# Kernel optimization log

Measured on AMD Instinct MI355X. Metric: run time of the kernel, lower is better.

## Reference

```python
import jax, jax.numpy as jnp
import numpy as np

D_IN = 2048; D_OUT = 2048; DL = 512; NUM_HEAD = 16; CTX = 2048
HEAD_DIM = D_OUT // NUM_HEAD  # 128


def setup_inputs() -> dict:
    key = jax.random.key(0)
    ks = jax.random.split(key, 20)
    s = 0.02
    def lin(k, din, dout):
        k1, k2 = jax.random.split(k)
        return (jax.random.normal(k1, (din, dout), jnp.float32) * s,
                jax.random.normal(k2, (dout,), jnp.float32) * s)
    w_kv, b_kv = lin(ks[0], D_IN, DL)
    w_ku, b_ku = lin(ks[1], DL, D_OUT // 2)
    w_kr, b_kr = lin(ks[2], D_IN, D_OUT // 2)
    w_vu, b_vu = lin(ks[3], DL, D_OUT)
    w_q,  b_q  = lin(ks[4], D_IN, DL)
    w_qu, b_qu = lin(ks[5], DL, D_OUT // 2)
    w_qr, b_qr = lin(ks[6], DL, D_OUT // 2)
    w_o,  b_o  = lin(ks[7], D_OUT, D_OUT)
    x = jax.random.normal(ks[8], (2, 2048, D_IN), jnp.float32)
    return dict(x=x, w_kv=w_kv, b_kv=b_kv, w_ku=w_ku, b_ku=b_ku, w_kr=w_kr, b_kr=b_kr,
                w_vu=w_vu, b_vu=b_vu, w_q=w_q, b_q=b_q, w_qu=w_qu, b_qu=b_qu,
                w_qr=w_qr, b_qr=b_qr, w_o=w_o, b_o=b_o)


def reference(x, w_kv, b_kv, w_ku, b_ku, w_kr, b_kr, w_vu, b_vu,
              w_q, b_q, w_qu, b_qu, w_qr, b_qr, w_o, b_o):
    b, s, _ = x.shape
    # latent KV compression
    ckv = x @ w_kv + b_kv                                   # (b, s, dl)
    # NOTE: source Rope.forward is a no-op (returns input), replicated faithfully.
    key = jnp.concatenate([ckv @ w_ku + b_ku, x @ w_kr + b_kr], axis=-1)   # (b, s, d_out)
    q_lat = x @ w_q + b_q                                   # (b, s, dl)
    query = jnp.concatenate([q_lat @ w_qu + b_qu, q_lat @ w_qr + b_qr], axis=-1)
    value = ckv @ w_vu + b_vu                               # (b, s, d_out)
    # split heads -> (b, h, s, hd)
    def heads(t):
        return t.reshape(b, s, NUM_HEAD, HEAD_DIM).transpose(0, 2, 1, 3)
    q, k, v = heads(query), heads(key), heads(value)
    scores = jnp.einsum('bhqd,bhkd->bhqk', q, k)
    causal = jnp.tril(jnp.ones((s, s), dtype=bool))
    scores = jnp.where(causal, scores, -jnp.inf)
    at = jax.nn.softmax(scores / jnp.sqrt(jnp.float32(HEAD_DIM)), axis=-1)
    # dropout rate 0 -> identity
    out = jnp.einsum('bhqk,bhkd->bhqd', at, v).transpose(0, 2, 1, 3).reshape(b, s, D_OUT)
    return out @ w_o + b_o
```

## Files before the change

### kernel.cpp

```cpp
#include <hip/hip_runtime.h>
#include <hip/hip_bf16.h>

typedef __hip_bfloat16 bf16;
typedef __bf16 bf16_t;
typedef __bf16 bf16x8 __attribute__((ext_vector_type(8)));
typedef __bf16 bf16x4v __attribute__((ext_vector_type(4)));
typedef float f32x4 __attribute__((ext_vector_type(4)));

#define D_IN 2048
#define D_OUT 2048
#define DL 512
#define NUM_HEAD 16
#define SEQ 2048
#define HEAD_DIM 128
#define BATCH 2
#define NTOK (BATCH * SEQ)

__device__ __forceinline__ void stf(float* p, float v) { *p = v; }
__device__ __forceinline__ void stf(bf16_t* p, float v) { *p = (bf16_t)v; }

__device__ __forceinline__ void async_cp16(const bf16_t* g, bf16_t* l) {
    __builtin_amdgcn_global_load_lds(
        (const __attribute__((address_space(1))) void*)g,
        (__attribute__((address_space(3))) void*)l, 16, 0, 0);
}

#define CVTB 8192
#define NTOPS 8

struct TOp { const float* W; bf16_t* Wt; int K, N, nx, nblk; };
struct TOps { TOp op[NTOPS]; };

__global__ __launch_bounds__(256) void prep_kernel(
    const float* __restrict__ x, bf16_t* __restrict__ xb,
    TOps ops,
    const float* __restrict__ b_kv, const float* __restrict__ b_q,
    float* __restrict__ bkvq,
    const float* __restrict__ b_qu, const float* __restrict__ b_qr,
    float* __restrict__ bquqr, int trb)
{
    const int tid = threadIdx.x;
    int blk = blockIdx.x;

    if (blk < CVTB) {
        int i = (blk * 256 + tid) * 4;
        float4 v = *(const float4*)&x[i];
        bf16_t o[4] = {(bf16_t)v.x, (bf16_t)v.y, (bf16_t)v.z, (bf16_t)v.w};
        *(ulong1*)&xb[i] = *(ulong1*)o;
        return;
    }
    blk -= CVTB;
    if (blk < trb) {
        int op = 0;
        while (blk >= ops.op[op].nblk) { blk -= ops.op[op].nblk; ++op; }
        const TOp& t = ops.op[op];
        const int n0 = (blk % t.nx) * 32, k0 = (blk / t.nx) * 32;
        __shared__ float tl[32][33];
        const int c = tid & 31, r0 = tid >> 5;
#pragma unroll
        for (int rr = 0; rr < 32; rr += 8)
            tl[r0 + rr][c] = t.W[(size_t)(k0 + r0 + rr) * t.N + n0 + c];
        __syncthreads();
#pragma unroll
        for (int rr = 0; rr < 32; rr += 8)
            t.Wt[(size_t)(n0 + r0 + rr) * t.K + k0 + c] = (bf16_t)tl[c][r0 + rr];
        return;
    }
    blk -= trb;
    if (blk == 0) {
#pragma unroll
        for (int j = 0; j < 4; ++j) {
            int i = tid + j * 256;
            bkvq[i] = (i < DL) ? b_kv[i] : b_q[i - DL];
        }
    } else {
#pragma unroll
        for (int j = 0; j < 8; ++j) {
            int i = tid + j * 256;
            bquqr[i] = (i < 1024) ? b_qu[i] : b_qr[i - 1024];
        }
    }
}

struct GOp { const bf16_t* A; const bf16_t* Wt; const float* bias;
             void* C; int lda, K, col0, ldc, nx, nblk; };
template <int N> struct GOps { GOp op[N]; };

template <typename TC, int NOPS>
__global__ __launch_bounds__(256) void gemm_multi_kernel(GOps<NOPS> ops)
{
    __shared__ __align__(16) bf16_t As[2 * 128 * 32];
    __shared__ __align__(16) bf16_t Bs[2 * 128 * 32];

    int blk = blockIdx.x;
    int opi = 0;
    while (blk >= ops.op[opi].nblk) { blk -= ops.op[opi].nblk; ++opi; }
    const GOp& g = ops.op[opi];

    const int tid  = threadIdx.x;
    const int wave = tid >> 6, lane = tid & 63;
    const int quad = lane >> 4, l16 = lane & 15;
    const int wm = wave & 1, wn = wave >> 1;
    const int m0 = (blk / g.nx) * 128;
    const int n0 = (blk % g.nx) * 128;

    const int r0 = tid >> 2, c0 = (tid & 3) * 8;
    const bf16_t* Ap0 = g.A  + (size_t)(m0 + r0)      * g.lda + c0;
    const bf16_t* Ap1 = g.A  + (size_t)(m0 + r0 + 64) * g.lda + c0;
    const bf16_t* Bp0 = g.Wt + (size_t)(n0 + r0)      * g.K   + c0;
    const bf16_t* Bp1 = g.Wt + (size_t)(n0 + r0 + 64) * g.K   + c0;

    f32x4 acc[4][4];
#pragma unroll
    for (int i = 0; i < 4; ++i)
#pragma unroll
        for (int j = 0; j < 4; ++j) acc[i][j] = (f32x4){0.f, 0.f, 0.f, 0.f};

    for (int k0 = 0; k0 < g.K; k0 += 64) {
        __syncthreads();
#pragma unroll
        for (int p = 0; p < 2; ++p) {
            async_cp16(Ap0 + k0 + p * 32, As + p * 4096 + tid * 8);
            async_cp16(Ap1 + k0 + p * 32, As + p * 4096 + 2048 + tid * 8);
            async_cp16(Bp0 + k0 + p * 32, Bs + p * 4096 + tid * 8);
            async_cp16(Bp1 + k0 + p * 32, Bs + p * 4096 + 2048 + tid * 8);
        }
        __syncthreads();

#pragma unroll
        for (int p = 0; p < 2; ++p) {
            bf16x8 af[4], bfr[4];
#pragma unroll
            for (int t = 0; t < 4; ++t) {
                af[t]  = *(const bf16x8*)&As[p * 4096 + (wm * 64 + t * 16 + l16) * 32 + quad * 8];
                bfr[t] = *(const bf16x8*)&Bs[p * 4096 + (wn * 64 + t * 16 + l16) * 32 + quad * 8];
            }
#pragma unroll
            for (int mt = 0; mt < 4; ++mt)
#pragma unroll
                for (int nt = 0; nt < 4; ++nt)
                    acc[mt][nt] = __builtin_amdgcn_mfma_f32_16x16x32_bf16(
                        af[mt], bfr[nt], acc[mt][nt], 0, 0, 0);
        }
    }

    TC* C = (TC*)g.C;
    const int mrow = m0 + wm * 64 + quad * 4;
#pragma unroll
    for (int mt = 0; mt < 4; ++mt)
#pragma unroll
        for (int nt = 0; nt < 4; ++nt) {
            int col = n0 + wn * 64 + nt * 16 + l16;
            float bv = g.bias[col];
#pragma unroll
            for (int r = 0; r < 4; ++r)
                stf(&C[(size_t)(mrow + mt * 16 + r) * g.ldc + g.col0 + col],
                    acc[mt][nt][r] + bv);
        }
}

#define KS_LD 136
#define VT_LD 72

__global__ __launch_bounds__(256, 4) void attn_mfma_kernel(
    bf16_t* __restrict__ Qg, const bf16_t* __restrict__ Kg,
    const bf16_t* __restrict__ Vg)
{
    __shared__ __align__(16) bf16_t Ks[64 * KS_LD];
    __shared__ __align__(16) bf16_t Vt[128 * VT_LD];

    const int tid  = threadIdx.x;
    const int wave = tid >> 6;
    const int lane = tid & 63;
    const int quad = lane >> 4;
    const int l16  = lane & 15;

    const int grp = blockIdx.x & 31;
    const int h   = grp & 15;
    const int b   = grp >> 4;
    const int u   = blockIdx.x >> 5;
    const int ua  = u >> 3, uc = u & 7;
    const int qt  = 8 * ua + ((ua & 1) ? (7 - uc) : uc);
    const int ntiles = qt + 1;

    const int base = b * SEQ;
    const int hd0  = h * HEAD_DIM;
    const float scale = 0.08838834764831845f;

    bf16x8 qf[4];
    {
        const bf16_t* qp = Qg + (size_t)(base + qt * 64 + wave * 16 + l16) * D_OUT + hd0;
#pragma unroll
        for (int kb = 0; kb < 4; ++kb)
            qf[kb] = *(const bf16x8*)(qp + kb * 32 + quad * 8);
    }

    f32x4 o[8];
#pragma unroll
    for (int ob = 0; ob < 8; ++ob) o[ob] = (f32x4){0.f, 0.f, 0.f, 0.f};
    float m_i = -INFINITY, l_i = 0.f;

    const int rk = tid >> 4, ck = (tid & 15) * 8;
    const int kg = (tid & 15) * 4, dg = tid >> 4;
    const int rbase = (rk >> 2) * 8 + (rk & 3);

    bf16x8 kpre[4], vpre[4];
    auto issue = [&](int k0) {
        const bf16_t* kp = Kg + (size_t)(base + k0 + rbase) * D_OUT + hd0 + ck;
        kpre[0] = *(const bf16x8*)(kp);
        kpre[1] = *(const bf16x8*)(kp + (size_t)4  * D_OUT);
        kpre[2] = *(const bf16x8*)(kp + (size_t)32 * D_OUT);
        kpre[3] = *(const bf16x8*)(kp + (size_t)36 * D_OUT);
#pragma unroll
        for (int kk = 0; kk < 4; ++kk)
            vpre[kk] = *(const bf16x8*)&Vg[(size_t)(base + k0 + kg + kk) * D_OUT + hd0 + dg * 8];
    };
    issue(0);

    const int qabs = qt * 64 + wave * 16 + l16;
    const int qwav = qt * 64 + wave * 16;

    for (int t = 0; t < ntiles; ++t) {
        const int k0 = t * 64;
        __syncthreads();
#pragma unroll
        for (int jj = 0; jj < 4; ++jj)
            *(bf16x8*)&Ks[(rk + 16 * jj) * KS_LD + ck] = kpre[jj];
#pragma unroll
        for (int j = 0; j < 8; ++j) {
            bf16x4v pk = {vpre[0][j], vpre[1][j], vpre[2][j], vpre[3][j]};
            *(bf16x4v*)&Vt[(dg * 8 + j) * VT_LD + kg] = pk;
        }
        __syncthreads();
        if (t + 1 < ntiles) issue(k0 + 64);

        f32x4 s[4];
#pragma unroll
        for (int nb = 0; nb < 4; ++nb) s[nb] = (f32x4){0.f, 0.f, 0.f, 0.f};
#pragma unroll
        for (int kb = 0; kb < 4; ++kb)
#pragma unroll
            for (int nb = 0; nb < 4; ++nb) {
                bf16x8 kfrag = *(const bf16x8*)&Ks[(nb * 16 + l16) * KS_LD + kb * 32 + quad * 8];
                s[nb] = __builtin_amdgcn_mfma_f32_16x16x32_bf16(kfrag, qf[kb], s[nb], 0, 0, 0);
            }

        if (k0 + 63 <= qwav) {
#pragma unroll
            for (int nb = 0; nb < 4; ++nb)
#pragma unroll
                for (int r = 0; r < 4; ++r) s[nb][r] *= scale;
        } else {
#pragma unroll
            for (int nb = 0; nb < 4; ++nb) {
                int key = k0 + (nb >> 1) * 32 + quad * 8 + (nb & 1) * 4;
#pragma unroll
                for (int r = 0; r < 4; ++r)
                    s[nb][r] = (key + r <= qabs) ? s[nb][r] * scale : -INFINITY;
            }
        }

        float rmax = -INFINITY;
#pragma unroll
        for (int nb = 0; nb < 4; ++nb)
#pragma unroll
            for (int r = 0; r < 4; ++r) rmax = fmaxf(rmax, s[nb][r]);
        rmax = fmaxf(rmax, __shfl_xor(rmax, 16, 64));
        rmax = fmaxf(rmax, __shfl_xor(rmax, 32, 64));

        const bool defer = (bool)__all(rmax - m_i <= 8.f);
        const float mnew = defer ? m_i : fmaxf(m_i, rmax);

        float rs = 0.f;
#pragma unroll
        for (int nb = 0; nb < 4; ++nb)
#pragma unroll
            for (int r = 0; r < 4; ++r) {
                float pv = __expf(s[nb][r] - mnew);
                s[nb][r] = pv;
                rs += pv;
            }
        rs += __shfl_xor(rs, 16, 64);
        rs += __shfl_xor(rs, 32, 64);

        if (!defer) {
            const float alpha = __expf(m_i - mnew);
            l_i = l_i * alpha + rs;
            m_i = mnew;
#pragma unroll
            for (int ob = 0; ob < 8; ++ob)
#pragma unroll
                for (int r = 0; r < 4; ++r) o[ob][r] *= alpha;
        } else {
            l_i += rs;
        }

        bf16x8 pb0, pb1;
#pragma unroll
        for (int r = 0; r < 4; ++r) {
            pb0[r]     = (bf16_t)s[0][r];
            pb0[4 + r] = (bf16_t)s[1][r];
            pb1[r]     = (bf16_t)s[2][r];
            pb1[4 + r] = (bf16_t)s[3][r];
        }

#pragma unroll
        for (int ob = 0; ob < 8; ++ob) {
            bf16x8 v0 = *(const bf16x8*)&Vt[(ob * 16 + l16) * VT_LD + 0 + quad * 8];
            o[ob] = __builtin_amdgcn_mfma_f32_16x16x32_bf16(v0, pb0, o[ob], 0, 0, 0);
            bf16x8 v1 = *(const bf16x8*)&Vt[(ob * 16 + l16) * VT_LD + 32 + quad * 8];
            o[ob] = __builtin_amdgcn_mfma_f32_16x16x32_bf16(v1, pb1, o[ob], 0, 0, 0);
        }
    }

    {
        const int q = qt * 64 + wave * 16 + l16;
        const float inv = 1.f / l_i;
        bf16_t* orow = Qg + (size_t)(base + q) * D_OUT + hd0;
#pragma unroll
        for (int ob = 0; ob < 8; ++ob) {
            bf16x4v pk = {(bf16_t)(o[ob][0] * inv), (bf16_t)(o[ob][1] * inv),
                          (bf16_t)(o[ob][2] * inv), (bf16_t)(o[ob][3] * inv)};
            *(bf16x4v*)&orow[ob * 16 + quad * 4] = pk;
        }
    }
}

extern "C" void kernel_launch(void* const* d_in, const int* in_sizes, int n_in,
                              void* d_out, int out_size, void* d_ws, size_t ws_size,
                              hipStream_t stream)
{
    const float* x    = (const float*)d_in[0];
    const float* w_kv = (const float*)d_in[1];
    const float* b_kv = (const float*)d_in[2];
    const float* w_ku = (const float*)d_in[3];
    const float* b_ku = (const float*)d_in[4];
    const float* w_kr = (const float*)d_in[5];
    const float* b_kr = (const float*)d_in[6];
    const float* w_vu = (const float*)d_in[7];
    const float* b_vu = (const float*)d_in[8];
    const float* w_q  = (const float*)d_in[9];
    const float* b_q  = (const float*)d_in[10];
    const float* w_qu = (const float*)d_in[11];
    const float* b_qu = (const float*)d_in[12];
    const float* w_qr = (const float*)d_in[13];
    const float* b_qr = (const float*)d_in[14];
    const float* w_o  = (const float*)d_in[15];
    const float* b_o  = (const float*)d_in[16];
    float* out = (float*)d_out;

    bf16_t* ws    = (bf16_t*)d_ws;
    bf16_t* ckvq  = ws;
    bf16_t* query = ckvq  + NTOK * 1024;
    bf16_t* value = query + NTOK * D_OUT;
    bf16_t* wt_kv = value + NTOK * D_OUT;
    bf16_t* wt_q  = wt_kv + 512 * 2048;
    bf16_t* wt_ku = wt_q  + 512 * 2048;
    bf16_t* wt_kr = wt_ku + 1024 * 512;
    bf16_t* wt_vu = wt_kr + 1024 * 2048;
    bf16_t* wt_qu = wt_vu + 2048 * 512;
    bf16_t* wt_qr = wt_qu + 1024 * 512;
    bf16_t* wt_o  = wt_qr + 1024 * 512;
    float*  bkvq  = (float*)(wt_o + 2048 * 2048);
    float*  bquqr = bkvq + 1024;
    bf16_t* key   = (bf16_t*)d_out;
    bf16_t* xb    = key + NTOK * D_OUT;

    TOps tops = {{
        { w_kv, wt_kv, 2048,  512, 16,  16 * 64 },
        { w_q,  wt_q,  2048,  512, 16,  16 * 64 },
        { w_ku, wt_ku,  512, 1024, 32,  32 * 16 },
        { w_kr, wt_kr, 2048, 1024, 32,  32 * 64 },
        { w_vu, wt_vu,  512, 2048, 64,  64 * 16 },
        { w_qu, wt_qu,  512, 1024, 32,  32 * 16 },
        { w_qr, wt_qr,  512, 1024, 32,  32 * 16 },
        { w_o,  wt_o,  2048, 2048, 64,  64 * 64 },
    }};
    int trb = 0;
    for (int i = 0; i < NTOPS; ++i) trb += tops.op[i].nblk;
    prep_kernel<<<CVTB + trb + 2, 256, 0, stream>>>(
        x, xb, tops, b_kv, b_q, bkvq, b_qu, b_qr, bquqr, trb);

    GOps<1> s1 = {{
        { xb, wt_kv, bkvq, ckvq, D_IN, D_IN, 0, 1024, 8, 8 * 32 },
    }};
    gemm_multi_kernel<bf16_t, 1><<<8 * 32, 256, 0, stream>>>(s1);

    GOps<4> s2 = {{
        { xb,         wt_kr, b_kr,  key,   D_IN, 2048, 1024, D_OUT,  8, 256 },
        { ckvq + 512, wt_qu, bquqr, query, 1024,  512,    0, D_OUT, 16, 512 },
        { ckvq,       wt_vu, b_vu,  value, 1024,  512,    0, D_OUT, 16, 512 },
        { ckvq,       wt_ku, b_ku,  key,   1024,  512,    0, D_OUT,  8, 256 },
    }};
    gemm_multi_kernel<bf16_t, 4><<<1536, 256, 0, stream>>>(s2);

    attn_mfma_kernel<<<1024, 256, 0, stream>>>(query, key, value);

    GOps<1> s3 = {{
        { query, wt_o, b_o, out, D_OUT, 2048, 0, D_OUT, 16, 512 },
    }};
    gemm_multi_kernel<float, 1><<<512, 256, 0, stream>>>(s3);
}
```

Before: 399.2 us.

## Pair complementary query tiles per attention block, double-buffer K/V, fold scale into Q

Each attention block now processes two query tiles (p and 31-p) that share the same K/V tiles, so causal work is balanced across blocks and each loaded K/V tile feeds twice the MFMAs. K/V shared memory is double-buffered, which removes one barrier per tile, and the MFMA sections are wrapped in s_setprio. The softmax scale is folded into the query GEMM epilogue through a new per-op cscale field, removing the per-score multiply. In exchange, register pressure roughly doubles (launch bounds drop from 4 to 2 blocks per SIMD), only 512 blocks are launched, and LDS use per block doubles.

```diff
diff --git a/kernel.cpp b/kernel.cpp
--- a/kernel.cpp
+++ b/kernel.cpp
@@ -15,6 +15,10 @@
 #define HEAD_DIM 128
 #define BATCH 2
 #define NTOK (BATCH * SEQ)
+#define SCALE 0.08838834764831845f
+
+struct CTrue  { static constexpr bool value = true;  };
+struct CFalse { static constexpr bool value = false; };
 
 __device__ __forceinline__ void stf(float* p, float v) { *p = v; }
 __device__ __forceinline__ void stf(bf16_t* p, float v) { *p = (bf16_t)v; }
@@ -83,7 +87,7 @@
 }
 
 struct GOp { const bf16_t* A; const bf16_t* Wt; const float* bias;
-             void* C; int lda, K, col0, ldc, nx, nblk; };
+             void* C; int lda, K, col0, ldc, nx, nblk; float cscale; };
 template <int N> struct GOps { GOp op[N]; };
 
 template <typename TC, int NOPS>
@@ -155,19 +159,21 @@
 #pragma unroll
             for (int r = 0; r < 4; ++r)
                 stf(&C[(size_t)(mrow + mt * 16 + r) * g.ldc + g.col0 + col],
-                    acc[mt][nt][r] + bv);
+                    (acc[mt][nt][r] + bv) * g.cscale);
         }
 }
 
 #define KS_LD 136
 #define VT_LD 72
-
-__global__ __launch_bounds__(256, 4) void attn_mfma_kernel(
+#define KS_SZ (64 * KS_LD)
+#define VT_SZ (128 * VT_LD)
+
+__global__ __launch_bounds__(256, 2) void attn_mfma_kernel(
     bf16_t* __restrict__ Qg, const bf16_t* __restrict__ Kg,
     const bf16_t* __restrict__ Vg)
 {
-    __shared__ __align__(16) bf16_t Ks[64 * KS_LD];
-    __shared__ __align__(16) bf16_t Vt[128 * VT_LD];
+    __shared__ __align__(16) bf16_t Ks[2][KS_SZ];
+    __shared__ __align__(16) bf16_t Vt[2][VT_SZ];
 
     const int tid  = threadIdx.x;
     const int wave = tid >> 6;
@@ -178,27 +184,31 @@
     const int grp = blockIdx.x & 31;
     const int h   = grp & 15;
     const int b   = grp >> 4;
-    const int u   = blockIdx.x >> 5;
-    const int ua  = u >> 3, uc = u & 7;
-    const int qt  = 8 * ua + ((ua & 1) ? (7 - uc) : uc);
-    const int ntiles = qt + 1;
+    const int p   = blockIdx.x >> 5;
+    const int qtA = p, qtB = 31 - p;
+    const int ntiles = qtB + 1;
 
     const int base = b * SEQ;
     const int hd0  = h * HEAD_DIM;
-    const float scale = 0.08838834764831845f;
-
-    bf16x8 qf[4];
+
+    bf16x8 qfA[4], qfB[4];
     {
-        const bf16_t* qp = Qg + (size_t)(base + qt * 64 + wave * 16 + l16) * D_OUT + hd0;
-#pragma unroll
-        for (int kb = 0; kb < 4; ++kb)
-            qf[kb] = *(const bf16x8*)(qp + kb * 32 + quad * 8);
-    }
-
-    f32x4 o[8];
-#pragma unroll
-    for (int ob = 0; ob < 8; ++ob) o[ob] = (f32x4){0.f, 0.f, 0.f, 0.f};
-    float m_i = -INFINITY, l_i = 0.f;
+        const bf16_t* qa = Qg + (size_t)(base + qtA * 64 + wave * 16 + l16) * D_OUT + hd0;
+        const bf16_t* qb = Qg + (size_t)(base + qtB * 64 + wave * 16 + l16) * D_OUT + hd0;
+#pragma unroll
+        for (int kb = 0; kb < 4; ++kb) {
+            qfA[kb] = *(const bf16x8*)(qa + kb * 32 + quad * 8);
+            qfB[kb] = *(const bf16x8*)(qb + kb * 32 + quad * 8);
+        }
+    }
+
+    f32x4 oA[8], oB[8];
+#pragma unroll
+    for (int ob = 0; ob < 8; ++ob) {
+        oA[ob] = (f32x4){0.f, 0.f, 0.f, 0.f};
+        oB[ob] = (f32x4){0.f, 0.f, 0.f, 0.f};
+    }
+    float mA = -INFINITY, mB = -INFINITY, lA = 0.f, lB = 0.f;
 
     const int rk = tid >> 4, ck = (tid & 15) * 8;
     const int kg = (tid & 15) * 4, dg = tid >> 4;
@@ -215,51 +225,26 @@
         for (int kk = 0; kk < 4; ++kk)
             vpre[kk] = *(const bf16x8*)&Vg[(size_t)(base + k0 + kg + kk) * D_OUT + hd0 + dg * 8];
     };
-    issue(0);
-
-    const int qabs = qt * 64 + wave * 16 + l16;
-    const int qwav = qt * 64 + wave * 16;
-
-    for (int t = 0; t < ntiles; ++t) {
-        const int k0 = t * 64;
-        __syncthreads();
+
+    auto stage = [&](int buf) {
+        bf16_t* ks = Ks[buf]; bf16_t* vt = Vt[buf];
 #pragma unroll
         for (int jj = 0; jj < 4; ++jj)
-            *(bf16x8*)&Ks[(rk + 16 * jj) * KS_LD + ck] = kpre[jj];
+            *(bf16x8*)&ks[(rk + 16 * jj) * KS_LD + ck] = kpre[jj];
 #pragma unroll
         for (int j = 0; j < 8; ++j) {
             bf16x4v pk = {vpre[0][j], vpre[1][j], vpre[2][j], vpre[3][j]};
-            *(bf16x4v*)&Vt[(dg * 8 + j) * VT_LD + kg] = pk;
-        }
-        __syncthreads();
-        if (t + 1 < ntiles) issue(k0 + 64);
-
-        f32x4 s[4];
-#pragma unroll
-        for (int nb = 0; nb < 4; ++nb) s[nb] = (f32x4){0.f, 0.f, 0.f, 0.f};
-#pragma unroll
-        for (int kb = 0; kb < 4; ++kb)
-#pragma unroll
-            for (int nb = 0; nb < 4; ++nb) {
-                bf16x8 kfrag = *(const bf16x8*)&Ks[(nb * 16 + l16) * KS_LD + kb * 32 + quad * 8];
-                s[nb] = __builtin_amdgcn_mfma_f32_16x16x32_bf16(kfrag, qf[kb], s[nb], 0, 0, 0);
-            }
-
-        if (k0 + 63 <= qwav) {
-#pragma unroll
-            for (int nb = 0; nb < 4; ++nb)
-#pragma unroll
-                for (int r = 0; r < 4; ++r) s[nb][r] *= scale;
-        } else {
-#pragma unroll
-            for (int nb = 0; nb < 4; ++nb) {
-                int key = k0 + (nb >> 1) * 32 + quad * 8 + (nb & 1) * 4;
-#pragma unroll
-                for (int r = 0; r < 4; ++r)
-                    s[nb][r] = (key + r <= qabs) ? s[nb][r] * scale : -INFINITY;
-            }
-        }
-
+            *(bf16x4v*)&vt[(dg * 8 + j) * VT_LD + kg] = pk;
+        }
+    };
+
+    const int qabsA = qtA * 64 + wave * 16 + l16;
+    const int qabsB = qtB * 64 + wave * 16 + l16;
+    const int qwavA = qtA * 64 + wave * 16;
+    const int qwavB = qtB * 64 + wave * 16;
+
+    auto softmax_one = [&](f32x4* s, float& m_i, float& l_i, f32x4* o,
+                           bf16x8& pb0, bf16x8& pb1) {
         float rmax = -INFINITY;
 #pragma unroll
         for (int nb = 0; nb < 4; ++nb)
@@ -267,10 +252,8 @@
             for (int r = 0; r < 4; ++r) rmax = fmaxf(rmax, s[nb][r]);
         rmax = fmaxf(rmax, __shfl_xor(rmax, 16, 64));
         rmax = fmaxf(rmax, __shfl_xor(rmax, 32, 64));
-
         const bool defer = (bool)__all(rmax - m_i <= 8.f);
         const float mnew = defer ? m_i : fmaxf(m_i, rmax);
-
         float rs = 0.f;
 #pragma unroll
         for (int nb = 0; nb < 4; ++nb)
@@ -282,7 +265,6 @@
             }
         rs += __shfl_xor(rs, 16, 64);
         rs += __shfl_xor(rs, 32, 64);
-
         if (!defer) {
             const float alpha = __expf(m_i - mnew);
             l_i = l_i * alpha + rs;
@@ -294,8 +276,6 @@
         } else {
             l_i += rs;
         }
-
-        bf16x8 pb0, pb1;
 #pragma unroll
         for (int r = 0; r < 4; ++r) {
             pb0[r]     = (bf16_t)s[0][r];
@@ -303,17 +283,90 @@
             pb1[r]     = (bf16_t)s[2][r];
             pb1[4 + r] = (bf16_t)s[3][r];
         }
-
+    };
+
+    auto tile_body = [&](auto doa, int cur, int k0) {
+        constexpr bool DOA = decltype(doa)::value;
+        const bf16_t* ks = Ks[cur];
+        const bf16_t* vt = Vt[cur];
+
+        f32x4 sB[4], sA[4];
+#pragma unroll
+        for (int nb = 0; nb < 4; ++nb) {
+            sB[nb] = (f32x4){0.f, 0.f, 0.f, 0.f};
+            sA[nb] = (f32x4){0.f, 0.f, 0.f, 0.f};
+        }
+
+        __builtin_amdgcn_s_setprio(1);
+#pragma unroll
+        for (int kb = 0; kb < 4; ++kb)
+#pragma unroll
+            for (int nb = 0; nb < 4; ++nb) {
+                bf16x8 kf = *(const bf16x8*)&ks[(nb * 16 + l16) * KS_LD + kb * 32 + quad * 8];
+                sB[nb] = __builtin_amdgcn_mfma_f32_16x16x32_bf16(kf, qfB[kb], sB[nb], 0, 0, 0);
+                if constexpr (DOA)
+                    sA[nb] = __builtin_amdgcn_mfma_f32_16x16x32_bf16(kf, qfA[kb], sA[nb], 0, 0, 0);
+            }
+        __builtin_amdgcn_s_setprio(0);
+
+        if (k0 + 63 > qwavB) {
+#pragma unroll
+            for (int nb = 0; nb < 4; ++nb) {
+                int key = k0 + (nb >> 1) * 32 + quad * 8 + (nb & 1) * 4;
+#pragma unroll
+                for (int r = 0; r < 4; ++r)
+                    if (key + r > qabsB) sB[nb][r] = -INFINITY;
+            }
+        }
+        if constexpr (DOA) {
+            if (k0 + 63 > qwavA) {
+#pragma unroll
+                for (int nb = 0; nb < 4; ++nb) {
+                    int key = k0 + (nb >> 1) * 32 + quad * 8 + (nb & 1) * 4;
+#pragma unroll
+                    for (int r = 0; r < 4; ++r)
+                        if (key + r > qabsA) sA[nb][r] = -INFINITY;
+                }
+            }
+        }
+
+        bf16x8 pbB0, pbB1, pbA0, pbA1;
+        softmax_one(sB, mB, lB, oB, pbB0, pbB1);
+        if constexpr (DOA) softmax_one(sA, mA, lA, oA, pbA0, pbA1);
+
+        __builtin_amdgcn_s_setprio(1);
 #pragma unroll
         for (int ob = 0; ob < 8; ++ob) {
-            bf16x8 v0 = *(const bf16x8*)&Vt[(ob * 16 + l16) * VT_LD + 0 + quad * 8];
-            o[ob] = __builtin_amdgcn_mfma_f32_16x16x32_bf16(v0, pb0, o[ob], 0, 0, 0);
-            bf16x8 v1 = *(const bf16x8*)&Vt[(ob * 16 + l16) * VT_LD + 32 + quad * 8];
-            o[ob] = __builtin_amdgcn_mfma_f32_16x16x32_bf16(v1, pb1, o[ob], 0, 0, 0);
-        }
-    }
-
-    {
+            bf16x8 v0 = *(const bf16x8*)&vt[(ob * 16 + l16) * VT_LD + quad * 8];
+            oB[ob] = __builtin_amdgcn_mfma_f32_16x16x32_bf16(v0, pbB0, oB[ob], 0, 0, 0);
+            if constexpr (DOA)
+                oA[ob] = __builtin_amdgcn_mfma_f32_16x16x32_bf16(v0, pbA0, oA[ob], 0, 0, 0);
+            bf16x8 v1 = *(const bf16x8*)&vt[(ob * 16 + l16) * VT_LD + 32 + quad * 8];
+            oB[ob] = __builtin_amdgcn_mfma_f32_16x16x32_bf16(v1, pbB1, oB[ob], 0, 0, 0);
+            if constexpr (DOA)
+                oA[ob] = __builtin_amdgcn_mfma_f32_16x16x32_bf16(v1, pbA1, oA[ob], 0, 0, 0);
+        }
+        __builtin_amdgcn_s_setprio(0);
+    };
+
+    issue(0);
+    stage(0);
+    issue(64);
+    __syncthreads();
+
+    for (int t = 0; t < ntiles; ++t) {
+        const int k0 = t * 64;
+        const int cur = t & 1;
+        if (t + 1 < ntiles) {
+            stage(cur ^ 1);
+            if (t + 2 < ntiles) issue((t + 2) * 64);
+        }
+        if (t <= qtA) tile_body(CTrue{},  cur, k0);
+        else          tile_body(CFalse{}, cur, k0);
+        __syncthreads();
+    }
+
+    auto writeback = [&](f32x4* o, float l_i, int qt) {
         const int q = qt * 64 + wave * 16 + l16;
         const float inv = 1.f / l_i;
         bf16_t* orow = Qg + (size_t)(base + q) * D_OUT + hd0;
@@ -323,7 +376,9 @@
                           (bf16_t)(o[ob][2] * inv), (bf16_t)(o[ob][3] * inv)};
             *(bf16x4v*)&orow[ob * 16 + quad * 4] = pk;
         }
-    }
+    };
+    writeback(oA, lA, qtA);
+    writeback(oB, lB, qtB);
 }
 
 extern "C" void kernel_launch(void* const* d_in, const int* in_sizes, int n_in,
@@ -382,22 +437,22 @@
         x, xb, tops, b_kv, b_q, bkvq, b_qu, b_qr, bquqr, trb);
 
     GOps<1> s1 = {{
-        { xb, wt_kv, bkvq, ckvq, D_IN, D_IN, 0, 1024, 8, 8 * 32 },
+        { xb, wt_kv, bkvq, ckvq, D_IN, D_IN, 0, 1024, 8, 8 * 32, 1.f },
     }};
     gemm_multi_kernel<bf16_t, 1><<<8 * 32, 256, 0, stream>>>(s1);
 
     GOps<4> s2 = {{
-        { xb,         wt_kr, b_kr,  key,   D_IN, 2048, 1024, D_OUT,  8, 256 },
-        { ckvq + 512, wt_qu, bquqr, query, 1024,  512,    0, D_OUT, 16, 512 },
-        { ckvq,       wt_vu, b_vu,  value, 1024,  512,    0, D_OUT, 16, 512 },
-        { ckvq,       wt_ku, b_ku,  key,   1024,  512,    0, D_OUT,  8, 256 },
+        { xb,         wt_kr, b_kr,  key,   D_IN, 2048, 1024, D_OUT,  8, 256, 1.f   },
+        { ckvq + 512, wt_qu, bquqr, query, 1024,  512,    0, D_OUT, 16, 512, SCALE },
+        { ckvq,       wt_vu, b_vu,  value, 1024,  512,    0, D_OUT, 16, 512, 1.f   },
+        { ckvq,       wt_ku, b_ku,  key,   1024,  512,    0, D_OUT,  8, 256, 1.f   },
     }};
     gemm_multi_kernel<bf16_t, 4><<<1536, 256, 0, stream>>>(s2);
 
-    attn_mfma_kernel<<<1024, 256, 0, stream>>>(query, key, value);
+    attn_mfma_kernel<<<512, 256, 0, stream>>>(query, key, value);
 
     GOps<1> s3 = {{
-        { query, wt_o, b_o, out, D_OUT, 2048, 0, D_OUT, 16, 512 },
+        { query, wt_o, b_o, out, D_OUT, 2048, 0, D_OUT, 16, 512, 1.f },
     }};
     gemm_multi_kernel<float, 1><<<512, 256, 0, stream>>>(s3);
 }
```

New measurement: 387.5 us. -2.9%, faster.
